# Performance work log

Hardware: AMD Instinct MI355X
Metric: run time of the kernel (lower is better)

Reference implementation:

```python
import jax, jax.numpy as jnp
import numpy as np

N = 100000
E = 1600000
VOCAB = 16
D = 128   # node_embedding_dim == hidden_channels
NUM_LAYERS = 3


def setup_inputs() -> dict:
    key = jax.random.key(0)
    ks = jax.random.split(key, 12)
    x = jax.random.randint(ks[0], (N, 1), 0, VOCAB, dtype=jnp.int64) if jax.config.jax_enable_x64 else jax.random.randint(ks[0], (N, 1), 0, VOCAB, dtype=jnp.int32)
    edge_index = jax.random.randint(ks[1], (2, E), 0, N, dtype=jnp.int32)
    s = 1.0 / np.sqrt(D)
    inp = {
        "x": x,
        "edge_index": edge_index,
        "emb": jax.random.normal(ks[2], (VOCAB, D), jnp.float32),
        "W0": jax.random.normal(ks[3], (D, D), jnp.float32) * s,
        "b0": jnp.zeros((D,), jnp.float32),
        "W1": jax.random.normal(ks[4], (D, D), jnp.float32) * s,
        "b1": jnp.zeros((D,), jnp.float32),
        "W2": jax.random.normal(ks[5], (D, D), jnp.float32) * s,
        "b2": jnp.zeros((D,), jnp.float32),
        "Wm1": jax.random.normal(ks[6], (2 * D, D), jnp.float32) * (1.0 / np.sqrt(2 * D)),
        "bm1": jnp.zeros((D,), jnp.float32),
        "Wm2": jax.random.normal(ks[7], (D, 3), jnp.float32) * s,
        "bm2": jnp.zeros((3,), jnp.float32),
    }
    return inp


def _gcn_conv(h, src_sl, dst_sl, norm, W, b):
    # PyG GCNConv: x' = scatter_dst(norm * (x W)[src]) + b, with self-loops included
    hW = h @ W                                   # [N, D]
    msg = hW[src_sl] * norm[:, None]             # [(E+N), D] gather
    agg = jax.ops.segment_sum(msg, dst_sl, num_segments=N)  # scatter-add
    return agg + b


def reference(x, edge_index, emb, W0, b0, W1, b1, W2, b2, Wm1, bm1, Wm2, bm2):
    src, dst = edge_index[0], edge_index[1]
    # add self-loops
    loop = jnp.arange(N, dtype=src.dtype)
    src_sl = jnp.concatenate([src, loop])
    dst_sl = jnp.concatenate([dst, loop])
    # symmetric degree normalization: deg counted on dst (col)
    deg = jax.ops.segment_sum(jnp.ones_like(dst_sl, jnp.float32), dst_sl, num_segments=N)
    dis = jnp.where(deg > 0, jax.lax.rsqrt(jnp.maximum(deg, 1.0)), 0.0)
    norm = dis[src_sl] * dis[dst_sl]             # [(E+N)]

    # node encoder: embedding lookup (dropout omitted: eval mode)
    h = emb[x[:, 0]]                             # [N, D]
    for W, b in ((W0, b0), (W1, b1), (W2, b2)):
        h = jax.nn.relu(_gcn_conv(h, src_sl, dst_sl, norm, W, b))

    # edge classifier: gather endpoints, concat, MLP
    ef = jnp.concatenate([h[src], h[dst]], axis=-1)   # [E, 2D]
    hid = jax.nn.relu(ef @ Wm1 + bm1)
    return hid @ Wm2 + bm2                             # [E, 3]
```

## Files before the change

kernel.cpp:

```cpp
#include <hip/hip_runtime.h>
#include <hip/hip_bf16.h>

#define N_NODES 100000
#define N_EDGES 1600000


__global__ void zero_cnt_k(int* cnt, int n) {
    int i = blockIdx.x * 256 + threadIdx.x;
    if (i < n) cnt[i] = 0;
}

__global__ void hist_k(const int* __restrict__ ei, int* __restrict__ cnt, int E) {
    int e = blockIdx.x * 256 + threadIdx.x;
    if (e < E) atomicAdd(&cnt[ei[E + e]], 1);
}

__global__ void scan_cnt_k(const int* __restrict__ cnt, const int* __restrict__ x,
                           int* __restrict__ offs, int* __restrict__ bsum,
                           float* __restrict__ dis, float2* __restrict__ sx, int n) {
    __shared__ int buf[2][256];
    int t = threadIdx.x;
    int i = blockIdx.x * 256 + t;
    int v = (i < n) ? cnt[i] : 0;
    if (i < n) {
        float d = rsqrtf(1.0f + (float)v);
        dis[i] = d;
        sx[i] = make_float2(d, __int_as_float(x[i]));
    }
    int p = 0;
    buf[0][t] = v;
    __syncthreads();
    for (int off = 1; off < 256; off <<= 1) {
        int nv = buf[p][t];
        if (t >= off) nv += buf[p][t - off];
        buf[p ^ 1][t] = nv;
        p ^= 1;
        __syncthreads();
    }
    if (i < n) offs[i] = buf[p][t] - v;
    if (t == 255) bsum[blockIdx.x] = buf[p][t];
}

__global__ void scan_bsum_k(int* __restrict__ bsum, int nb) {
    __shared__ int buf[2][512];
    int t = threadIdx.x;
    int v = (t < nb) ? bsum[t] : 0;
    int p = 0;
    buf[0][t] = v;
    __syncthreads();
    for (int off = 1; off < 512; off <<= 1) {
        int nv = buf[p][t];
        if (t >= off) nv += buf[p][t - off];
        buf[p ^ 1][t] = nv;
        p ^= 1;
        __syncthreads();
    }
    if (t < nb) bsum[t] = buf[p][t] - v;
}

__global__ void scan_add_k(int* __restrict__ offs, int* __restrict__ cursor,
                           const int* __restrict__ bsum, int n, int total) {
    int i = blockIdx.x * 256 + threadIdx.x;
    if (i < n) {
        int o = offs[i] + bsum[blockIdx.x];
        offs[i] = o;
        cursor[i] = o;
    }
    if (i == 0) offs[n] = total;
}

__global__ void fill_csr_k(const int* __restrict__ ei, int* __restrict__ cursor,
                           int* __restrict__ srcs, int* __restrict__ eid, int E) {
    int e = blockIdx.x * 256 + threadIdx.x;
    if (e < E) {
        int s = ei[e];
        int d = ei[E + e];
        int pos = atomicAdd(&cursor[d], 1);
        srcs[pos] = s;
        eid[pos] = e;
    }
}


__global__ void t0_k(const float* __restrict__ emb, const float* __restrict__ W0,
                     float* __restrict__ T0) {
    int v = blockIdx.x;
    int c = threadIdx.x;
    float acc = 0.f;
    for (int k = 0; k < 128; ++k) acc += emb[v * 128 + k] * W0[k * 128 + c];
    T0[v * 128 + c] = acc;
}

__global__ __launch_bounds__(256) void vgather_k(const float2* __restrict__ sx,
                                                 const int* __restrict__ offs,
                                                 const int* __restrict__ srcs,
                                                 const float* __restrict__ dis,
                                                 const int* __restrict__ x,
                                                 const float* __restrict__ T0,
                                                 const float* __restrict__ b0,
                                                 float* __restrict__ h, int n) {
    __shared__ float t0s[16 * 128];
    __shared__ float cv[4][16];
    int t = threadIdx.x;
    #pragma unroll
    for (int i = 0; i < 8; ++i) t0s[t + i * 256] = T0[t + i * 256];
    if (t < 64) cv[t >> 4][t & 15] = 0.f;
    __syncthreads();

    int w = t >> 6, lane = t & 63;
    int node = blockIdx.x * 4 + w;
    float di = dis[node];
    int j0 = offs[node], j1 = offs[node + 1];
    for (int j = j0 + lane; j < j1; j += 64) {
        float2 v = sx[srcs[j]];
        atomicAdd(&cv[w][__float_as_int(v.y)], v.x);
    }
    if (lane == 0) atomicAdd(&cv[w][x[node]], di);
    __syncthreads();

    float2 acc = make_float2(0.f, 0.f);
    #pragma unroll
    for (int v = 0; v < 16; ++v) {
        float c = cv[w][v];
        float2 tv = *(const float2*)&t0s[v * 128 + lane * 2];
        acc.x += c * tv.x;
        acc.y += c * tv.y;
    }
    float2 bb = *(const float2*)&b0[lane * 2];
    float2 r = make_float2(fmaxf(di * acc.x + bb.x, 0.f),
                           fmaxf(di * acc.y + bb.y, 0.f));
    ((float2*)h)[(size_t)node * 64 + lane] = r;
}


__global__ __launch_bounds__(256) void matmul128_k(const float* __restrict__ in,
                                                   const float* __restrict__ W,
                                                   float* __restrict__ out,
                                                   const float* __restrict__ scale,
                                                   int n) {
    __shared__ float hlds[64][132];
    int t = threadIdx.x;
    int row0 = blockIdx.x * 64;
    #pragma unroll
    for (int it = 0; it < 8; ++it) {
        int i4 = t + it * 256;
        int r = i4 >> 5, c4 = (i4 & 31) << 2;
        float4 v = make_float4(0.f, 0.f, 0.f, 0.f);
        int g = row0 + r;
        if (g < n) v = *(const float4*)&in[(size_t)g * 128 + c4];
        *(float4*)&hlds[r][c4] = v;
    }
    __syncthreads();
    int cg = t & 31, rg = t >> 5;
    int c0 = cg << 2;
    float acc[8][4];
    #pragma unroll
    for (int r = 0; r < 8; ++r)
        for (int j = 0; j < 4; ++j) acc[r][j] = 0.f;
    #pragma unroll 4
    for (int kc = 0; kc < 32; ++kc) {
        float4 w0 = *(const float4*)&W[(size_t)(4 * kc + 0) * 128 + c0];
        float4 w1 = *(const float4*)&W[(size_t)(4 * kc + 1) * 128 + c0];
        float4 w2 = *(const float4*)&W[(size_t)(4 * kc + 2) * 128 + c0];
        float4 w3 = *(const float4*)&W[(size_t)(4 * kc + 3) * 128 + c0];
        #pragma unroll
        for (int r = 0; r < 8; ++r) {
            float4 hv = *(const float4*)&hlds[rg * 8 + r][kc * 4];
            acc[r][0] += hv.x * w0.x + hv.y * w1.x + hv.z * w2.x + hv.w * w3.x;
            acc[r][1] += hv.x * w0.y + hv.y * w1.y + hv.z * w2.y + hv.w * w3.y;
            acc[r][2] += hv.x * w0.z + hv.y * w1.z + hv.z * w2.z + hv.w * w3.z;
            acc[r][3] += hv.x * w0.w + hv.y * w1.w + hv.z * w2.w + hv.w * w3.w;
        }
    }
    #pragma unroll
    for (int r = 0; r < 8; ++r) {
        int g = row0 + rg * 8 + r;
        if (g < n) {
            float sc = scale[g];
            float4 o = make_float4(acc[r][0] * sc, acc[r][1] * sc,
                                   acc[r][2] * sc, acc[r][3] * sc);
            *(float4*)&out[(size_t)g * 128 + c0] = o;
        }
    }
}

__global__ __launch_bounds__(256) void matmulAB_k(const float* __restrict__ in,
                                                  const float* __restrict__ WA,
                                                  const float* __restrict__ WB,
                                                  float* __restrict__ outA,
                                                  float* __restrict__ outB, int n) {
    __shared__ float hlds[64][132];
    int t = threadIdx.x;
    int row0 = blockIdx.x * 64;
    #pragma unroll
    for (int it = 0; it < 8; ++it) {
        int i4 = t + it * 256;
        int r = i4 >> 5, c4 = (i4 & 31) << 2;
        float4 v = make_float4(0.f, 0.f, 0.f, 0.f);
        int g = row0 + r;
        if (g < n) v = *(const float4*)&in[(size_t)g * 128 + c4];
        *(float4*)&hlds[r][c4] = v;
    }
    __syncthreads();
    int cg = t & 31, rg = t >> 5;
    int c0 = cg << 2;
    float accA[8][4], accB[8][4];
    #pragma unroll
    for (int r = 0; r < 8; ++r)
        for (int j = 0; j < 4; ++j) { accA[r][j] = 0.f; accB[r][j] = 0.f; }
    #pragma unroll 2
    for (int kc = 0; kc < 32; ++kc) {
        float4 wa0 = *(const float4*)&WA[(size_t)(4 * kc + 0) * 128 + c0];
        float4 wa1 = *(const float4*)&WA[(size_t)(4 * kc + 1) * 128 + c0];
        float4 wa2 = *(const float4*)&WA[(size_t)(4 * kc + 2) * 128 + c0];
        float4 wa3 = *(const float4*)&WA[(size_t)(4 * kc + 3) * 128 + c0];
        float4 wb0 = *(const float4*)&WB[(size_t)(4 * kc + 0) * 128 + c0];
        float4 wb1 = *(const float4*)&WB[(size_t)(4 * kc + 1) * 128 + c0];
        float4 wb2 = *(const float4*)&WB[(size_t)(4 * kc + 2) * 128 + c0];
        float4 wb3 = *(const float4*)&WB[(size_t)(4 * kc + 3) * 128 + c0];
        #pragma unroll
        for (int r = 0; r < 8; ++r) {
            float4 hv = *(const float4*)&hlds[rg * 8 + r][kc * 4];
            accA[r][0] += hv.x * wa0.x + hv.y * wa1.x + hv.z * wa2.x + hv.w * wa3.x;
            accA[r][1] += hv.x * wa0.y + hv.y * wa1.y + hv.z * wa2.y + hv.w * wa3.y;
            accA[r][2] += hv.x * wa0.z + hv.y * wa1.z + hv.z * wa2.z + hv.w * wa3.z;
            accA[r][3] += hv.x * wa0.w + hv.y * wa1.w + hv.z * wa2.w + hv.w * wa3.w;
            accB[r][0] += hv.x * wb0.x + hv.y * wb1.x + hv.z * wb2.x + hv.w * wb3.x;
            accB[r][1] += hv.x * wb0.y + hv.y * wb1.y + hv.z * wb2.y + hv.w * wb3.y;
            accB[r][2] += hv.x * wb0.z + hv.y * wb1.z + hv.z * wb2.z + hv.w * wb3.z;
            accB[r][3] += hv.x * wb0.w + hv.y * wb1.w + hv.z * wb2.w + hv.w * wb3.w;
        }
    }
    #pragma unroll
    for (int r = 0; r < 8; ++r) {
        int g = row0 + rg * 8 + r;
        if (g < n) {
            *(float4*)&outA[(size_t)g * 128 + c0] = *(float4*)&accA[r][0];
            *(float4*)&outB[(size_t)g * 128 + c0] = *(float4*)&accB[r][0];
        }
    }
}

__global__ __launch_bounds__(256) void gcn_gather_k(const float* __restrict__ hW,
                                                    const int* __restrict__ offs,
                                                    const int* __restrict__ srcs,
                                                    const float* __restrict__ dis,
                                                    const float* __restrict__ bias,
                                                    float* __restrict__ hout, int n) {
    int t = threadIdx.x;
    int node = blockIdx.x * 4 + (t >> 6);
    int lane = t & 63;
    int g = lane >> 3, sl = lane & 7;
    const float4* hw4 = (const float4*)hW;
    size_t selfrb = (size_t)node * 32 + sl;
    float4 a[4];
    if (g == 0) {
        #pragma unroll
        for (int k = 0; k < 4; ++k) a[k] = hw4[selfrb + 8 * k];
    } else {
        #pragma unroll
        for (int k = 0; k < 4; ++k) a[k] = make_float4(0.f, 0.f, 0.f, 0.f);
    }
    int j0 = offs[node], j1 = offs[node + 1];
    for (int j = j0 + g; j < j1; j += 8) {
        size_t rb = (size_t)srcs[j] * 32 + sl;
        #pragma unroll
        for (int k = 0; k < 4; ++k) {
            float4 u = hw4[rb + 8 * k];
            a[k].x += u.x; a[k].y += u.y; a[k].z += u.z; a[k].w += u.w;
        }
    }
    #pragma unroll
    for (int m = 8; m <= 32; m <<= 1) {
        #pragma unroll
        for (int k = 0; k < 4; ++k) {
            a[k].x += __shfl_xor(a[k].x, m);
            a[k].y += __shfl_xor(a[k].y, m);
            a[k].z += __shfl_xor(a[k].z, m);
            a[k].w += __shfl_xor(a[k].w, m);
        }
    }
    if (g == 0) {
        float di = dis[node];
        #pragma unroll
        for (int k = 0; k < 4; ++k) {
            float4 bb = ((const float4*)bias)[sl + 8 * k];
            float4 r = make_float4(fmaxf(di * a[k].x + bb.x, 0.f),
                                   fmaxf(di * a[k].y + bb.y, 0.f),
                                   fmaxf(di * a[k].z + bb.z, 0.f),
                                   fmaxf(di * a[k].w + bb.w, 0.f));
            ((float4*)hout)[selfrb + 8 * k] = r;
        }
    }
}

__global__ __launch_bounds__(256) void edge_mlp_k(const int* __restrict__ offs,
                                                  const int* __restrict__ srcs,
                                                  const int* __restrict__ eid,
                                                  const float* __restrict__ A,
                                                  const float* __restrict__ B,
                                                  const float* __restrict__ Wm2,
                                                  const float* __restrict__ bm1,
                                                  const float* __restrict__ bm2,
                                                  float* __restrict__ out, int n) {
    int t = threadIdx.x;
    int node = blockIdx.x * 4 + (t >> 6);
    int lane = t & 63;
    int g = lane >> 4, sl = lane & 15;
    int j0 = offs[node], j1 = offs[node + 1];
    if (j0 == j1) return;

    const float4* B4 = (const float4*)(B + (size_t)node * 128 + sl * 8);
    const float4* bm14 = (const float4*)(bm1 + sl * 8);
    float4 pre0 = B4[0], pre1 = B4[1];
    float4 m0 = bm14[0], m1 = bm14[1];
    pre0.x += m0.x; pre0.y += m0.y; pre0.z += m0.z; pre0.w += m0.w;
    pre1.x += m1.x; pre1.y += m1.y; pre1.z += m1.z; pre1.w += m1.w;

    float wv[8][3];
    #pragma unroll
    for (int i = 0; i < 8; ++i) {
        int f = sl * 8 + i;
        wv[i][0] = Wm2[f * 3 + 0];
        wv[i][1] = Wm2[f * 3 + 1];
        wv[i][2] = Wm2[f * 3 + 2];
    }
    float c0 = bm2[0], c1 = bm2[1], c2 = bm2[2];

    for (int jb = j0; jb < j1; jb += 4) {
        int jj = jb + g;
        bool act = jj < j1;
        int jsafe = act ? jj : j0;
        int s = srcs[jsafe];
        int e = eid[jsafe];
        const float4* A4 = (const float4*)(A + (size_t)s * 128 + sl * 8);
        float4 a0 = A4[0], a1 = A4[1];
        float h[8];
        h[0] = fmaxf(a0.x + pre0.x, 0.f);
        h[1] = fmaxf(a0.y + pre0.y, 0.f);
        h[2] = fmaxf(a0.z + pre0.z, 0.f);
        h[3] = fmaxf(a0.w + pre0.w, 0.f);
        h[4] = fmaxf(a1.x + pre1.x, 0.f);
        h[5] = fmaxf(a1.y + pre1.y, 0.f);
        h[6] = fmaxf(a1.z + pre1.z, 0.f);
        h[7] = fmaxf(a1.w + pre1.w, 0.f);
        float p0 = 0.f, p1 = 0.f, p2 = 0.f;
        #pragma unroll
        for (int i = 0; i < 8; ++i) {
            p0 += h[i] * wv[i][0];
            p1 += h[i] * wv[i][1];
            p2 += h[i] * wv[i][2];
        }
        #pragma unroll
        for (int m = 1; m <= 8; m <<= 1) {
            p0 += __shfl_xor(p0, m);
            p1 += __shfl_xor(p1, m);
            p2 += __shfl_xor(p2, m);
        }
        if (act && sl == 0) {
            out[(size_t)e * 3 + 0] = p0 + c0;
            out[(size_t)e * 3 + 1] = p1 + c1;
            out[(size_t)e * 3 + 2] = p2 + c2;
        }
    }
}

extern "C" void kernel_launch(void* const* d_in, const int* in_sizes, int n_in,
                              void* d_out, int out_size, void* d_ws, size_t ws_size,
                              hipStream_t stream) {
    const int N = N_NODES, E = N_EDGES;
    const int* x    = (const int*)d_in[0];
    const int* ei   = (const int*)d_in[1];
    const float* emb = (const float*)d_in[2];
    const float* W0 = (const float*)d_in[3];
    const float* b0 = (const float*)d_in[4];
    const float* W1 = (const float*)d_in[5];
    const float* b1 = (const float*)d_in[6];
    const float* W2 = (const float*)d_in[7];
    const float* b2 = (const float*)d_in[8];
    const float* Wm1 = (const float*)d_in[9];
    const float* bm1 = (const float*)d_in[10];
    const float* Wm2 = (const float*)d_in[11];
    const float* bm2 = (const float*)d_in[12];
    float* out = (float*)d_out;

    char* p = (char*)d_ws;
    auto alloc = [&](size_t bytes) {
        char* r = p;
        p += (bytes + 511) & ~(size_t)511;
        return r;
    };
    int*    cnt    = (int*)alloc((size_t)N * 4);
    float*  dis    = (float*)alloc((size_t)N * 4);
    float2* sx     = (float2*)alloc((size_t)N * 8);
    int*    offs   = (int*)alloc((size_t)(N + 1) * 4);
    int*    cursor = (int*)alloc((size_t)N * 4);
    int*    bsum   = (int*)alloc(512 * 4);
    int*    srcs   = (int*)alloc((size_t)E * 4);
    int*    eid    = (int*)alloc((size_t)E * 4);
    float*  T0     = (float*)alloc(16 * 128 * 4);
    float*  buf0   = (float*)alloc((size_t)N * 128 * 4);
    float*  buf1   = (float*)alloc((size_t)N * 128 * 4);
    float*  buf2   = (float*)alloc((size_t)N * 128 * 4);

    int nbN = (N + 255) / 256;
    int nbE = (E + 255) / 256;
    int nodeBlocks = N / 4;
    int mmBlocks = (N + 63) / 64;

    zero_cnt_k<<<nbN, 256, 0, stream>>>(cnt, N);
    hist_k<<<nbE, 256, 0, stream>>>(ei, cnt, E);
    scan_cnt_k<<<nbN, 256, 0, stream>>>(cnt, x, offs, bsum, dis, sx, N);
    scan_bsum_k<<<1, 512, 0, stream>>>(bsum, nbN);
    scan_add_k<<<nbN, 256, 0, stream>>>(offs, cursor, bsum, N, E);
    fill_csr_k<<<nbE, 256, 0, stream>>>(ei, cursor, srcs, eid, E);

    t0_k<<<16, 128, 0, stream>>>(emb, W0, T0);
    vgather_k<<<nodeBlocks, 256, 0, stream>>>(sx, offs, srcs, dis, x, T0, b0, buf0, N);

    const float* Ws[2] = {W1, W2};
    const float* bs[2] = {b1, b2};
    for (int l = 0; l < 2; ++l) {
        matmul128_k<<<mmBlocks, 256, 0, stream>>>(buf0, Ws[l], buf1, dis, N);
        gcn_gather_k<<<nodeBlocks, 256, 0, stream>>>(buf1, offs, srcs, dis, bs[l], buf0, N);
    }

    matmulAB_k<<<mmBlocks, 256, 0, stream>>>(buf0, Wm1, Wm1 + 128 * 128, buf1, buf2, N);

    edge_mlp_k<<<nodeBlocks, 256, 0, stream>>>(offs, srcs, eid, buf1, buf2, Wm2, bm1, bm2, out, N);
}
```

Baseline: 854.1 us.

## Pack degree scale and vocab id into one int; simplify matmul k-loops

Packs the per-node degree scale and the vocabulary id into a single 32-bit word by masking off the low 4 mantissa bits, so the first-layer gather reads 4 bytes per neighbor instead of 8. The packing slightly perturbs the scale values. The zeroing kernel is replaced with hipMemsetAsync. The two node matmul kernels now step k one at a time with scalar LDS reads and a single weight float4 per step, instead of four rows of weights per step, which changes the mix of instructions and register use.

```diff
diff --git a/kernel.cpp b/kernel.cpp
--- a/kernel.cpp
+++ b/kernel.cpp
@@ -4,11 +4,6 @@
 #define N_NODES 100000
 #define N_EDGES 1600000
 
-
-__global__ void zero_cnt_k(int* cnt, int n) {
-    int i = blockIdx.x * 256 + threadIdx.x;
-    if (i < n) cnt[i] = 0;
-}
 
 __global__ void hist_k(const int* __restrict__ ei, int* __restrict__ cnt, int E) {
     int e = blockIdx.x * 256 + threadIdx.x;
@@ -17,7 +12,7 @@
 
 __global__ void scan_cnt_k(const int* __restrict__ cnt, const int* __restrict__ x,
                            int* __restrict__ offs, int* __restrict__ bsum,
-                           float* __restrict__ dis, float2* __restrict__ sx, int n) {
+                           float* __restrict__ dis, int* __restrict__ sxp, int n) {
     __shared__ int buf[2][256];
     int t = threadIdx.x;
     int i = blockIdx.x * 256 + t;
@@ -25,7 +20,7 @@
     if (i < n) {
         float d = rsqrtf(1.0f + (float)v);
         dis[i] = d;
-        sx[i] = make_float2(d, __int_as_float(x[i]));
+        sxp[i] = (__float_as_int(d) & ~15) | x[i];
     }
     int p = 0;
     buf[0][t] = v;
@@ -91,11 +86,10 @@
     T0[v * 128 + c] = acc;
 }
 
-__global__ __launch_bounds__(256) void vgather_k(const float2* __restrict__ sx,
+__global__ __launch_bounds__(256) void vgather_k(const int* __restrict__ sxp,
                                                  const int* __restrict__ offs,
                                                  const int* __restrict__ srcs,
                                                  const float* __restrict__ dis,
-                                                 const int* __restrict__ x,
                                                  const float* __restrict__ T0,
                                                  const float* __restrict__ b0,
                                                  float* __restrict__ h, int n) {
@@ -112,10 +106,10 @@
     float di = dis[node];
     int j0 = offs[node], j1 = offs[node + 1];
     for (int j = j0 + lane; j < j1; j += 64) {
-        float2 v = sx[srcs[j]];
-        atomicAdd(&cv[w][__float_as_int(v.y)], v.x);
-    }
-    if (lane == 0) atomicAdd(&cv[w][x[node]], di);
+        int b = sxp[srcs[j]];
+        atomicAdd(&cv[w][b & 15], __int_as_float(b));
+    }
+    if (lane == 0) atomicAdd(&cv[w][sxp[node] & 15], di);
     __syncthreads();
 
     float2 acc = make_float2(0.f, 0.f);
@@ -158,18 +152,15 @@
     for (int r = 0; r < 8; ++r)
         for (int j = 0; j < 4; ++j) acc[r][j] = 0.f;
     #pragma unroll 4
-    for (int kc = 0; kc < 32; ++kc) {
-        float4 w0 = *(const float4*)&W[(size_t)(4 * kc + 0) * 128 + c0];
-        float4 w1 = *(const float4*)&W[(size_t)(4 * kc + 1) * 128 + c0];
-        float4 w2 = *(const float4*)&W[(size_t)(4 * kc + 2) * 128 + c0];
-        float4 w3 = *(const float4*)&W[(size_t)(4 * kc + 3) * 128 + c0];
+    for (int k = 0; k < 128; ++k) {
+        float4 w = *(const float4*)&W[(size_t)k * 128 + c0];
         #pragma unroll
         for (int r = 0; r < 8; ++r) {
-            float4 hv = *(const float4*)&hlds[rg * 8 + r][kc * 4];
-            acc[r][0] += hv.x * w0.x + hv.y * w1.x + hv.z * w2.x + hv.w * w3.x;
-            acc[r][1] += hv.x * w0.y + hv.y * w1.y + hv.z * w2.y + hv.w * w3.y;
-            acc[r][2] += hv.x * w0.z + hv.y * w1.z + hv.z * w2.z + hv.w * w3.z;
-            acc[r][3] += hv.x * w0.w + hv.y * w1.w + hv.z * w2.w + hv.w * w3.w;
+            float hk = hlds[rg * 8 + r][k];
+            acc[r][0] += hk * w.x;
+            acc[r][1] += hk * w.y;
+            acc[r][2] += hk * w.z;
+            acc[r][3] += hk * w.w;
         }
     }
     #pragma unroll
@@ -209,26 +200,20 @@
     for (int r = 0; r < 8; ++r)
         for (int j = 0; j < 4; ++j) { accA[r][j] = 0.f; accB[r][j] = 0.f; }
     #pragma unroll 2
-    for (int kc = 0; kc < 32; ++kc) {
-        float4 wa0 = *(const float4*)&WA[(size_t)(4 * kc + 0) * 128 + c0];
-        float4 wa1 = *(const float4*)&WA[(size_t)(4 * kc + 1) * 128 + c0];
-        float4 wa2 = *(const float4*)&WA[(size_t)(4 * kc + 2) * 128 + c0];
-        float4 wa3 = *(const float4*)&WA[(size_t)(4 * kc + 3) * 128 + c0];
-        float4 wb0 = *(const float4*)&WB[(size_t)(4 * kc + 0) * 128 + c0];
-        float4 wb1 = *(const float4*)&WB[(size_t)(4 * kc + 1) * 128 + c0];
-        float4 wb2 = *(const float4*)&WB[(size_t)(4 * kc + 2) * 128 + c0];
-        float4 wb3 = *(const float4*)&WB[(size_t)(4 * kc + 3) * 128 + c0];
+    for (int k = 0; k < 128; ++k) {
+        float4 wa = *(const float4*)&WA[(size_t)k * 128 + c0];
+        float4 wb = *(const float4*)&WB[(size_t)k * 128 + c0];
         #pragma unroll
         for (int r = 0; r < 8; ++r) {
-            float4 hv = *(const float4*)&hlds[rg * 8 + r][kc * 4];
-            accA[r][0] += hv.x * wa0.x + hv.y * wa1.x + hv.z * wa2.x + hv.w * wa3.x;
-            accA[r][1] += hv.x * wa0.y + hv.y * wa1.y + hv.z * wa2.y + hv.w * wa3.y;
-            accA[r][2] += hv.x * wa0.z + hv.y * wa1.z + hv.z * wa2.z + hv.w * wa3.z;
-            accA[r][3] += hv.x * wa0.w + hv.y * wa1.w + hv.z * wa2.w + hv.w * wa3.w;
-            accB[r][0] += hv.x * wb0.x + hv.y * wb1.x + hv.z * wb2.x + hv.w * wb3.x;
-            accB[r][1] += hv.x * wb0.y + hv.y * wb1.y + hv.z * wb2.y + hv.w * wb3.y;
-            accB[r][2] += hv.x * wb0.z + hv.y * wb1.z + hv.z * wb2.z + hv.w * wb3.z;
-            accB[r][3] += hv.x * wb0.w + hv.y * wb1.w + hv.z * wb2.w + hv.w * wb3.w;
+            float hk = hlds[rg * 8 + r][k];
+            accA[r][0] += hk * wa.x;
+            accA[r][1] += hk * wa.y;
+            accA[r][2] += hk * wa.z;
+            accA[r][3] += hk * wa.w;
+            accB[r][0] += hk * wb.x;
+            accB[r][1] += hk * wb.y;
+            accB[r][2] += hk * wb.z;
+            accB[r][3] += hk * wb.w;
         }
     }
     #pragma unroll
@@ -392,7 +377,7 @@
     };
     int*    cnt    = (int*)alloc((size_t)N * 4);
     float*  dis    = (float*)alloc((size_t)N * 4);
-    float2* sx     = (float2*)alloc((size_t)N * 8);
+    int*    sxp    = (int*)alloc((size_t)N * 4);
     int*    offs   = (int*)alloc((size_t)(N + 1) * 4);
     int*    cursor = (int*)alloc((size_t)N * 4);
     int*    bsum   = (int*)alloc(512 * 4);
@@ -408,15 +393,15 @@
     int nodeBlocks = N / 4;
     int mmBlocks = (N + 63) / 64;
 
-    zero_cnt_k<<<nbN, 256, 0, stream>>>(cnt, N);
+    hipMemsetAsync(cnt, 0, (size_t)N * 4, stream);
     hist_k<<<nbE, 256, 0, stream>>>(ei, cnt, E);
-    scan_cnt_k<<<nbN, 256, 0, stream>>>(cnt, x, offs, bsum, dis, sx, N);
+    scan_cnt_k<<<nbN, 256, 0, stream>>>(cnt, x, offs, bsum, dis, sxp, N);
     scan_bsum_k<<<1, 512, 0, stream>>>(bsum, nbN);
     scan_add_k<<<nbN, 256, 0, stream>>>(offs, cursor, bsum, N, E);
     fill_csr_k<<<nbE, 256, 0, stream>>>(ei, cursor, srcs, eid, E);
 
     t0_k<<<16, 128, 0, stream>>>(emb, W0, T0);
-    vgather_k<<<nodeBlocks, 256, 0, stream>>>(sx, offs, srcs, dis, x, T0, b0, buf0, N);
+    vgather_k<<<nodeBlocks, 256, 0, stream>>>(sxp, offs, srcs, dis, T0, b0, buf0, N);
 
     const float* Ws[2] = {W1, W2};
     const float* bs[2] = {b1, b2};
```

New measurement: 812.6 us. 4.9% less time.
